# Kernel optimization log

Hardware: AMD Instinct MI355X
Metric: run time of the kernel (lower is better)

The kernel has to match this reference:

```python
import jax, jax.numpy as jnp
import numpy as np

N, E, IN_CH, HID, HEADS, OUT = 50000, 400000, 256, 128, 4, 2
EPS = 1e-5

def _bn(x, g, b):
    # training-mode BatchNorm1d (biased variance), dropout treated as eval (off)
    m = jnp.mean(x, axis=0)
    v = jnp.mean((x - m) ** 2, axis=0)
    return (x - m) * jax.lax.rsqrt(v + EPS) * g + b

def _sage(x, src, dst, Wl, bl, Wr):
    # PyG SAGEConv: lin_l(mean_{j->i} x_j) + lin_r(x_i)
    msg = jax.ops.segment_sum(x[src], dst, num_segments=N)
    deg = jax.ops.segment_sum(jnp.ones((src.shape[0],), x.dtype), dst, num_segments=N)
    agg = msg / jnp.maximum(deg, 1.0)[:, None]
    return agg @ Wl.T + bl + x @ Wr.T

def _gat(x, src, dst, W, a_s, a_d, bias):
    # PyG GATConv with self-loops already appended to (src, dst); concat heads
    d = W.shape[0] // HEADS
    xh = (x @ W.T).reshape(N, HEADS, d)
    asrc = jnp.einsum('nhd,hd->nh', xh, a_s)
    adst = jnp.einsum('nhd,hd->nh', xh, a_d)
    e = jax.nn.leaky_relu(asrc[src] + adst[dst], 0.2)          # [E+N, H]
    m = jax.ops.segment_max(e, dst, num_segments=N)            # segment softmax
    ex = jnp.exp(e - m[dst])
    den = jax.ops.segment_sum(ex, dst, num_segments=N)
    alpha = ex / den[dst]
    out = jax.ops.segment_sum(alpha[:, :, None] * xh[src], dst, num_segments=N)
    return out.reshape(N, HEADS * d) + bias

def setup_inputs():
    key = jax.random.key(0)
    ks = jax.random.split(key, 12)
    rnd = lambda k, s: jax.random.normal(k, s, dtype=jnp.float32) * 0.05
    H4 = HID * HEADS
    return {
        'x': jax.random.normal(ks[0], (N, IN_CH), dtype=jnp.float32),
        'edge_index': jax.random.randint(ks[1], (2, E), 0, N, dtype=jnp.int32),
        'W1l': rnd(ks[2], (HID, IN_CH)), 'b1': jnp.zeros((HID,), jnp.float32),
        'W1r': rnd(ks[3], (HID, IN_CH)),
        'g1': jnp.ones((HID,), jnp.float32), 'be1': jnp.zeros((HID,), jnp.float32),
        'Wg': rnd(ks[4], (H4, HID)),
        'a_src': rnd(ks[5], (HEADS, HID)), 'a_dst': rnd(ks[6], (HEADS, HID)),
        'gbias': jnp.zeros((H4,), jnp.float32),
        'g2': jnp.ones((H4,), jnp.float32), 'be2': jnp.zeros((H4,), jnp.float32),
        'W2l': rnd(ks[7], (HID, H4)), 'b2': jnp.zeros((HID,), jnp.float32),
        'W2r': rnd(ks[8], (HID, H4)),
        'g3': jnp.ones((HID,), jnp.float32), 'be3': jnp.zeros((HID,), jnp.float32),
        'Wf1': rnd(ks[9], (HID // 2, HID)), 'bf1': jnp.zeros((HID // 2,), jnp.float32),
        'g4': jnp.ones((HID // 2,), jnp.float32), 'be4': jnp.zeros((HID // 2,), jnp.float32),
        'Wf2': rnd(ks[10], (OUT, HID // 2)), 'bf2': jnp.zeros((OUT,), jnp.float32),
    }

def reference(x, edge_index, W1l, b1, W1r, g1, be1, Wg, a_src, a_dst, gbias,
              g2, be2, W2l, b2, W2r, g3, be3, Wf1, bf1, g4, be4, Wf2, bf2):
    src, dst = edge_index[0], edge_index[1]
    h = jax.nn.elu(_bn(_sage(x, src, dst, W1l, b1, W1r), g1, be1))
    loop = jnp.arange(N, dtype=src.dtype)                      # GAT adds self-loops
    src_sl = jnp.concatenate([src, loop])
    dst_sl = jnp.concatenate([dst, loop])
    h = jax.nn.elu(_bn(_gat(h, src_sl, dst_sl, Wg, a_src, a_dst, gbias), g2, be2))
    h = jax.nn.elu(_bn(_sage(h, src, dst, W2l, b2, W2r), g3, be3))
    h = jax.nn.elu(_bn(h @ Wf1.T + bf1, g4, be4))
    return h @ Wf2.T + bf2
```

## Files before the change

kernel.cpp:

```cpp
#include <hip/hip_runtime.h>
#include <cstdint>
#include <cstddef>

#define NN 50000
#define EE 400000
#define BN_EPS 1e-5f
#define NB_SCAN 196
#define NWAVE 8192
#define GB 784
#define GAGG 2048
#define G2 64

typedef __attribute__((ext_vector_type(8))) short s16x8;
typedef __attribute__((ext_vector_type(4))) float floatx4;

__device__ __forceinline__ unsigned short f2b(float f) {
    uint32_t u = __float_as_uint(f);
    uint32_t r = (u + 0x7fffu + ((u >> 16) & 1u)) >> 16;
    return (unsigned short)r;
}
__device__ __forceinline__ uint32_t pack2(float a, float b) {
    return (uint32_t)f2b(a) | ((uint32_t)f2b(b) << 16);
}
__device__ __forceinline__ float b2f_lo(uint32_t u) { return __uint_as_float(u << 16); }
__device__ __forceinline__ float b2f_hi(uint32_t u) { return __uint_as_float(u & 0xffff0000u); }

#define GLD16(g, l) __builtin_amdgcn_global_load_lds(                          \
    (const __attribute__((address_space(1))) uint32_t*)(g),                    \
    (__attribute__((address_space(3))) uint32_t*)(l), 16, 0, 0)

__global__ __launch_bounds__(256)
void gemm_w256(const unsigned short* __restrict__ A,
               const unsigned short* __restrict__ W,
               unsigned short* __restrict__ Cb, float* __restrict__ Cf,
               int M, int K)
{
    __shared__ __align__(16) unsigned short As[128 * 32];
    __shared__ __align__(16) unsigned short Bs[256 * 32];
    const int t  = threadIdx.x;
    const int m0 = blockIdx.x * 128;
    const int lane = t & 63;
    const int lr = lane & 15;
    const int lq = lane >> 4;
    const int wid = t >> 6;
    const int wr  = (wid >> 1) * 64;
    const int wc2 = (wid & 1) * 128;

    floatx4 acc[4][8];
    const floatx4 zero = {0.f, 0.f, 0.f, 0.f};
    #pragma unroll
    for (int i = 0; i < 4; ++i)
        #pragma unroll
        for (int j = 0; j < 8; ++j) acc[i][j] = zero;

    for (int k0 = 0; k0 < K; k0 += 32) {
        #pragma unroll
        for (int it = 0; it < 2; ++it) {
            const int seg  = t + it * 256;
            const int row  = seg >> 2;
            const int klog = (seg & 3) ^ ((row >> 1) & 3);
            const unsigned short* ga = A + (size_t)min(m0 + row, M - 1) * K + k0 + klog * 8;
            GLD16(ga, As + seg * 8);
        }
        #pragma unroll
        for (int it = 0; it < 4; ++it) {
            const int seg  = t + it * 256;
            const int row  = seg >> 2;
            const int klog = (seg & 3) ^ ((row >> 1) & 3);
            const unsigned short* gb = W + (size_t)row * K + k0 + klog * 8;
            GLD16(gb, Bs + seg * 8);
        }
        __syncthreads();

        s16x8 af[4], bf[8];
        #pragma unroll
        for (int i = 0; i < 4; ++i) {
            const int ra = wr + i * 16 + lr;
            const int pa = lq ^ ((ra >> 1) & 3);
            af[i] = *(const s16x8*)(As + (ra * 4 + pa) * 8);
        }
        #pragma unroll
        for (int j = 0; j < 8; ++j) {
            const int rb = wc2 + j * 16 + lr;
            const int pb = lq ^ ((rb >> 1) & 3);
            bf[j] = *(const s16x8*)(Bs + (rb * 4 + pb) * 8);
        }
        #pragma unroll
        for (int i = 0; i < 4; ++i)
            #pragma unroll
            for (int j = 0; j < 8; ++j)
                acc[i][j] = __builtin_amdgcn_mfma_f32_16x16x32_bf16(
                    bf[j], af[i], acc[i][j], 0, 0, 0);
        __syncthreads();
    }

    const int orow = lane & 15;
    const int oc4  = (lane >> 4) * 4;
    #pragma unroll
    for (int i = 0; i < 4; ++i) {
        const int r = m0 + wr + i * 16 + orow;
        if (r >= M) continue;
        if (wc2 == 0) {
            #pragma unroll
            for (int j = 0; j < 8; ++j) {
                const int c = j * 16 + oc4;
                const floatx4 a = acc[i][j];
                uint2 ov;
                ov.x = pack2(a[0], a[1]);
                ov.y = pack2(a[2], a[3]);
                *(uint2*)(Cb + (size_t)r * 128 + c) = ov;
            }
        } else {
            #pragma unroll
            for (int j = 0; j < 8; ++j) {
                const int c = j * 16 + oc4;
                const floatx4 a = acc[i][j];
                *(float4*)(Cf + (size_t)r * 128 + c) = make_float4(a[0], a[1], a[2], a[3]);
            }
        }
    }
}

__global__ __launch_bounds__(256)
void gemm_bf16mm(const unsigned short* __restrict__ A,
                 const unsigned short* __restrict__ W,
                 const float* __restrict__ bias,
                 unsigned short* __restrict__ Cb, float* __restrict__ Cf,
                 int split, int M, int K, int Ncol, int ldb, int ldf)
{
    __shared__ __align__(16) unsigned short As[128 * 32];
    __shared__ __align__(16) unsigned short Bs[128 * 32];
    const int t  = threadIdx.x;
    const int m0 = blockIdx.y * 128;
    const int n0 = blockIdx.x * 128;
    const int lane = t & 63;
    const int lr = lane & 15;
    const int lq = lane >> 4;
    const int wr = (t >> 7) * 64;
    const int wc = ((t >> 6) & 1) * 64;

    floatx4 acc[4][4];
    const floatx4 zero = {0.f, 0.f, 0.f, 0.f};
    #pragma unroll
    for (int i = 0; i < 4; ++i)
        #pragma unroll
        for (int j = 0; j < 4; ++j) acc[i][j] = zero;

    for (int k0 = 0; k0 < K; k0 += 32) {
        #pragma unroll
        for (int it = 0; it < 2; ++it) {
            const int seg  = t + it * 256;
            const int row  = seg >> 2;
            const int klog = (seg & 3) ^ ((row >> 1) & 3);
            const unsigned short* ga = A + (size_t)min(m0 + row, M - 1) * K + k0 + klog * 8;
            GLD16(ga, As + seg * 8);
            const unsigned short* gb = W + (size_t)min(n0 + row, Ncol - 1) * K + k0 + klog * 8;
            GLD16(gb, Bs + seg * 8);
        }
        __syncthreads();

        s16x8 af[4], bf[4];
        #pragma unroll
        for (int i = 0; i < 4; ++i) {
            const int ra = wr + i * 16 + lr;
            const int pa = lq ^ ((ra >> 1) & 3);
            af[i] = *(const s16x8*)(As + (ra * 4 + pa) * 8);
            const int rb = wc + i * 16 + lr;
            const int pb = lq ^ ((rb >> 1) & 3);
            bf[i] = *(const s16x8*)(Bs + (rb * 4 + pb) * 8);
        }
        #pragma unroll
        for (int i = 0; i < 4; ++i)
            #pragma unroll
            for (int j = 0; j < 4; ++j)
                acc[i][j] = __builtin_amdgcn_mfma_f32_16x16x32_bf16(
                    bf[j], af[i], acc[i][j], 0, 0, 0);
        __syncthreads();
    }

    const int orow = lane & 15;
    const int oc4  = (lane >> 4) * 4;
    #pragma unroll
    for (int i = 0; i < 4; ++i) {
        const int r = m0 + wr + i * 16 + orow;
        if (r >= M) continue;
        #pragma unroll
        for (int j = 0; j < 4; ++j) {
            const int cb = n0 + wc + j * 16 + oc4;
            if (cb >= Ncol) continue;
            const floatx4 a = acc[i][j];
            if (cb < split) {
                uint2 ov;
                ov.x = pack2(a[0], a[1]);
                ov.y = pack2(a[2], a[3]);
                *(uint2*)(Cb + (size_t)r * ldb + cb) = ov;
            } else {
                const int cc = cb - split;
                float4 o = make_float4(a[0], a[1], a[2], a[3]);
                if (bias) {
                    o.x += bias[cc]; o.y += bias[cc + 1];
                    o.z += bias[cc + 2]; o.w += bias[cc + 3];
                }
                *(float4*)(Cf + (size_t)r * ldf + cc) = o;
            }
        }
    }
}

__global__ __launch_bounds__(256)
void gemm_heads(const unsigned short* __restrict__ agg,
                const unsigned short* __restrict__ Wg,
                const float* __restrict__ gbias,
                unsigned short* __restrict__ out)
{
    __shared__ __align__(16) unsigned short As[128 * 32];
    __shared__ __align__(16) unsigned short Bs[128 * 32];
    const int t  = threadIdx.x;
    const int m0 = blockIdx.x * 128;
    const int h  = blockIdx.y;
    const int lane = t & 63;
    const int lr = lane & 15;
    const int lq = lane >> 4;
    const int wr = (t >> 7) * 64;
    const int wc = ((t >> 6) & 1) * 64;

    floatx4 acc[4][4];
    const floatx4 zero = {0.f, 0.f, 0.f, 0.f};
    #pragma unroll
    for (int i = 0; i < 4; ++i)
        #pragma unroll
        for (int j = 0; j < 4; ++j) acc[i][j] = zero;

    for (int k0 = 0; k0 < 128; k0 += 32) {
        #pragma unroll
        for (int it = 0; it < 2; ++it) {
            const int seg  = t + it * 256;
            const int row  = seg >> 2;
            const int klog = (seg & 3) ^ ((row >> 1) & 3);
            const unsigned short* ga = agg + (size_t)min(m0 + row, NN - 1) * 512 + h * 128 + k0 + klog * 8;
            GLD16(ga, As + seg * 8);
            const unsigned short* gb = Wg + (size_t)(h * 128 + row) * 128 + k0 + klog * 8;
            GLD16(gb, Bs + seg * 8);
        }
        __syncthreads();

        s16x8 af[4], bf[4];
        #pragma unroll
        for (int i = 0; i < 4; ++i) {
            const int ra = wr + i * 16 + lr;
            const int pa = lq ^ ((ra >> 1) & 3);
            af[i] = *(const s16x8*)(As + (ra * 4 + pa) * 8);
            const int rb = wc + i * 16 + lr;
            const int pb = lq ^ ((rb >> 1) & 3);
            bf[i] = *(const s16x8*)(Bs + (rb * 4 + pb) * 8);
        }
        #pragma unroll
        for (int i = 0; i < 4; ++i)
            #pragma unroll
            for (int j = 0; j < 4; ++j)
                acc[i][j] = __builtin_amdgcn_mfma_f32_16x16x32_bf16(
                    bf[j], af[i], acc[i][j], 0, 0, 0);
        __syncthreads();
    }

    const int orow = lane & 15;
    const int oc4  = (lane >> 4) * 4;
    #pragma unroll
    for (int i = 0; i < 4; ++i) {
        const int r = m0 + wr + i * 16 + orow;
        if (r >= NN) continue;
        #pragma unroll
        for (int j = 0; j < 4; ++j) {
            const int c = wc + j * 16 + oc4;
            const floatx4 a = acc[i][j];
            const float* gb = gbias + h * 128 + c;
            uint2 ov;
            ov.x = pack2(a[0] + gb[0], a[1] + gb[1]);
            ov.y = pack2(a[2] + gb[2], a[3] + gb[3]);
            *(uint2*)(out + (size_t)r * 512 + h * 128 + c) = ov;
        }
    }
}

__global__ void k_conv_x(const float* __restrict__ x, unsigned short* __restrict__ xb)
{
    const int i8 = (blockIdx.x * 256 + threadIdx.x) * 8;
    const float4 f0 = *(const float4*)(x + i8);
    const float4 f1 = *(const float4*)(x + i8 + 4);
    uint4 o;
    o.x = pack2(f0.x, f0.y); o.y = pack2(f0.z, f0.w);
    o.z = pack2(f1.x, f1.y); o.w = pack2(f1.z, f1.w);
    *(uint4*)(xb + i8) = o;
}

__global__ void k_conv_w(const float* __restrict__ s0, const float* __restrict__ s1,
                         const float* __restrict__ s2, const float* __restrict__ s3,
                         const float* __restrict__ s4, const float* __restrict__ s5,
                         unsigned short* __restrict__ dst)
{
    const int i = blockIdx.x * 256 + threadIdx.x;
    if (i >= 270336) return;
    float v;
    if      (i < 32768)  v = s0[i];
    else if (i < 65536)  v = s1[i - 32768];
    else if (i < 131072) v = s2[i - 65536];
    else if (i < 196608) v = s3[i - 131072];
    else if (i < 262144) v = s4[i - 196608];
    else                 v = s5[i - 262144];
    dst[i] = f2b(v);
}

__global__ void k_atilde(const float* __restrict__ a_s, const float* __restrict__ a_d,
                         const float* __restrict__ Wg, float* __restrict__ ats,
                         float* __restrict__ atd)
{
    const int k = threadIdx.x;
    const int h = blockIdx.x;
    float s = 0.f, d = 0.f;
    for (int j = 0; j < 128; ++j) {
        const float w = Wg[(size_t)(h * 128 + j) * 128 + k];
        s += a_s[h * 128 + j] * w;
        d += a_d[h * 128 + j] * w;
    }
    ats[h * 128 + k] = s;
    atd[h * 128 + k] = d;
}

__global__ void k_count(const int* __restrict__ dst, int* __restrict__ cnt)
{
    int i = blockIdx.x * blockDim.x + threadIdx.x;
    if (i < EE) atomicAdd(&cnt[dst[i]], 1);
}

__global__ __launch_bounds__(256)
void k_scan_blk(const int* __restrict__ cnt, int* __restrict__ offs,
                int* __restrict__ bsum, int N)
{
    __shared__ int wsum[4];
    const int t = threadIdx.x;
    const int i = blockIdx.x * 256 + t;
    const int v = (i < N) ? cnt[i] : 0;
    int s = v;
    #pragma unroll
    for (int o = 1; o < 64; o <<= 1) {
        const int u = __shfl_up(s, o);
        if ((t & 63) >= o) s += u;
    }
    const int wid = t >> 6;
    if ((t & 63) == 63) wsum[wid] = s;
    __syncthreads();
    int base = 0;
    #pragma unroll
    for (int w = 0; w < 3; ++w) if (w < wid) base += wsum[w];
    if (i < N) offs[i] = base + s - v;
    if (t == 255) bsum[blockIdx.x] = base + s;
}

__global__ __launch_bounds__(256)
void k_scan_top(int* __restrict__ bsum, int* __restrict__ offs, int N)
{
    __shared__ int wsum[4];
    const int t = threadIdx.x;
    const int v = (t < NB_SCAN) ? bsum[t] : 0;
    int s = v;
    #pragma unroll
    for (int o = 1; o < 64; o <<= 1) {
        const int u = __shfl_up(s, o);
        if ((t & 63) >= o) s += u;
    }
    const int wid = t >> 6;
    if ((t & 63) == 63) wsum[wid] = s;
    __syncthreads();
    int base = 0;
    #pragma unroll
    for (int w = 0; w < 3; ++w) if (w < wid) base += wsum[w];
    if (t < NB_SCAN) bsum[t] = base + s - v;
    if (t == 255) offs[N] = base + s;
}

__global__ __launch_bounds__(256)
void k_scan_add(int* __restrict__ offs, const int* __restrict__ bsum, int N)
{
    const int i = blockIdx.x * 256 + threadIdx.x;
    if (i < N) offs[i] += bsum[blockIdx.x];
}

__global__ void k_fill(const int* __restrict__ src, const int* __restrict__ dst,
                       const int* __restrict__ offs, int* __restrict__ fill,
                       int* __restrict__ csr)
{
    int i = blockIdx.x * blockDim.x + threadIdx.x;
    if (i < EE) {
        int d = dst[i];
        int p = offs[d] + atomicAdd(&fill[d], 1);
        csr[p] = src[i];
    }
}

__global__ __launch_bounds__(256)
void k_sage_agg(const unsigned short* __restrict__ tl, float* __restrict__ tr,
                const float* __restrict__ bias, const int* __restrict__ offs,
                const int* __restrict__ csr, float* __restrict__ P)
{
    __shared__ float red[4][256];
    const int l  = threadIdx.x & 63;
    const int g  = l >> 4;
    const int c0 = (l & 15) * 8;
    const int wid = threadIdx.x >> 6;
    const int wv = blockIdx.x * 4 + wid;
    const float4 bv0 = *(const float4*)(bias + c0);
    const float4 bv1 = *(const float4*)(bias + c0 + 4);
    float ps[8] = {0.f,0.f,0.f,0.f,0.f,0.f,0.f,0.f};
    float qs[8] = {0.f,0.f,0.f,0.f,0.f,0.f,0.f,0.f};
    for (int nb = wv * 4; nb < NN; nb += NWAVE * 4) {
        const int n = nb + g;
        if (n < NN) {
            const int o0 = offs[n];
            const int deg = offs[n + 1] - o0;
            float a[8] = {0.f,0.f,0.f,0.f,0.f,0.f,0.f,0.f};
            for (int j = 0; j < deg; ++j) {
                const int sid = csr[o0 + j];
                const uint4 q = *(const uint4*)(tl + (size_t)sid * 128 + c0);
                a[0] += b2f_lo(q.x); a[1] += b2f_hi(q.x);
                a[2] += b2f_lo(q.y); a[3] += b2f_hi(q.y);
                a[4] += b2f_lo(q.z); a[5] += b2f_hi(q.z);
                a[6] += b2f_lo(q.w); a[7] += b2f_hi(q.w);
            }
            const float inv = 1.f / fmaxf((float)deg, 1.f);
            float* tp = tr + (size_t)n * 128 + c0;
            float4 t0 = *(float4*)tp;
            float4 t1 = *(float4*)(tp + 4);
            float v[8];
            v[0] = t0.x + a[0] * inv + bv0.x; v[1] = t0.y + a[1] * inv + bv0.y;
            v[2] = t0.z + a[2] * inv + bv0.z; v[3] = t0.w + a[3] * inv + bv0.w;
            v[4] = t1.x + a[4] * inv + bv1.x; v[5] = t1.y + a[5] * inv + bv1.y;
            v[6] = t1.z + a[6] * inv + bv1.z; v[7] = t1.w + a[7] * inv + bv1.w;
            *(float4*)tp       = make_float4(v[0], v[1], v[2], v[3]);
            *(float4*)(tp + 4) = make_float4(v[4], v[5], v[6], v[7]);
            #pragma unroll
            for (int i = 0; i < 8; ++i) { ps[i] += v[i]; qs[i] += v[i] * v[i]; }
        }
    }
    #pragma unroll
    for (int i = 0; i < 8; ++i) {
        ps[i] += __shfl_xor(ps[i], 16); ps[i] += __shfl_xor(ps[i], 32);
        qs[i] += __shfl_xor(qs[i], 16); qs[i] += __shfl_xor(qs[i], 32);
    }
    if (l < 16) {
        #pragma unroll
        for (int i = 0; i < 8; ++i) {
            red[wid][c0 + i]       = ps[i];
            red[wid][128 + c0 + i] = qs[i];
        }
    }
    __syncthreads();
    const int tc = threadIdx.x;
    const float s = red[0][tc] + red[1][tc] + red[2][tc] + red[3][tc];
    P[(size_t)blockIdx.x * 256 + tc] = s;
}

__global__ __launch_bounds__(256)
void k_attn_agg(const unsigned short* __restrict__ h1, const float* __restrict__ asrc,
                const float* __restrict__ adst, const int* __restrict__ offs,
                const int* __restrict__ csr, unsigned short* __restrict__ agg)
{
    const int l  = threadIdx.x & 63;
    const int g  = l >> 4;
    const int c0 = (l & 15) * 8;
    const int wv = blockIdx.x * 4 + (threadIdx.x >> 6);
    for (int nb = wv * 4; nb < NN; nb += NWAVE * 4) {
        const int n = nb + g;
        if (n >= NN) continue;
        const int o0 = offs[n];
        const int deg = offs[n + 1] - o0;
        const int total = deg + 1;
        const float4 adv = *(const float4*)(adst + n * 4);
        float den0 = 0.f, den1 = 0.f, den2 = 0.f, den3 = 0.f;
        float acc[4][8];
        #pragma unroll
        for (int h = 0; h < 4; ++h)
            #pragma unroll
            for (int i = 0; i < 8; ++i) acc[h][i] = 0.f;
        for (int j = 0; j < total; ++j) {
            const int sid = (j < deg) ? csr[o0 + j] : n;
            const float4 av = *(const float4*)(asrc + sid * 4);
            float e0 = av.x + adv.x, e1 = av.y + adv.y;
            float e2 = av.z + adv.z, e3 = av.w + adv.w;
            e0 = fmaxf(e0, 0.2f * e0); e1 = fmaxf(e1, 0.2f * e1);
            e2 = fmaxf(e2, 0.2f * e2); e3 = fmaxf(e3, 0.2f * e3);
            const float w0 = __expf(e0), w1 = __expf(e1);
            const float w2 = __expf(e2), w3 = __expf(e3);
            den0 += w0; den1 += w1; den2 += w2; den3 += w3;
            const uint4 q = *(const uint4*)(h1 + (size_t)sid * 128 + c0);
            float v[8];
            v[0] = b2f_lo(q.x); v[1] = b2f_hi(q.x);
            v[2] = b2f_lo(q.y); v[3] = b2f_hi(q.y);
            v[4] = b2f_lo(q.z); v[5] = b2f_hi(q.z);
            v[6] = b2f_lo(q.w); v[7] = b2f_hi(q.w);
            #pragma unroll
            for (int i = 0; i < 8; ++i) {
                acc[0][i] += w0 * v[i];
                acc[1][i] += w1 * v[i];
                acc[2][i] += w2 * v[i];
                acc[3][i] += w3 * v[i];
            }
        }
        const float r[4] = {1.f / den0, 1.f / den1, 1.f / den2, 1.f / den3};
        #pragma unroll
        for (int h = 0; h < 4; ++h) {
            uint4 ov;
            ov.x = pack2(acc[h][0] * r[h], acc[h][1] * r[h]);
            ov.y = pack2(acc[h][2] * r[h], acc[h][3] * r[h]);
            ov.z = pack2(acc[h][4] * r[h], acc[h][5] * r[h]);
            ov.w = pack2(acc[h][6] * r[h], acc[h][7] * r[h]);
            *(uint4*)(agg + (size_t)n * 512 + h * 128 + c0) = ov;
        }
    }
}

__global__ __launch_bounds__(256)
void k_statsA_b2(const unsigned short* __restrict__ X, float* __restrict__ P)
{
    const int c = threadIdx.x * 2;
    const int b = blockIdx.x;
    const int r0 = b * 64;
    const int r1 = min(r0 + 64, NN);
    float s0 = 0.f, s1 = 0.f, q0 = 0.f, q1 = 0.f;
    for (int r = r0; r < r1; ++r) {
        const uint32_t u = *(const uint32_t*)(X + (size_t)r * 512 + c);
        const float v0 = b2f_lo(u), v1 = b2f_hi(u);
        s0 += v0; q0 += v0 * v0;
        s1 += v1; q1 += v1 * v1;
    }
    *(float2*)(P + (size_t)b * 1024 + c) = make_float2(s0, s1);
    *(float2*)(P + (size_t)b * 1024 + 512 + c) = make_float2(q0, q1);
}

__global__ __launch_bounds__(64)
void k_statsA_f(const float* __restrict__ X, float* __restrict__ P)
{
    const int c = threadIdx.x;
    const int b = blockIdx.x;
    const int r0 = b * 64;
    const int r1 = min(r0 + 64, NN);
    float s = 0.f, q = 0.f;
    for (int r = r0; r < r1; ++r) {
        const float v = X[(size_t)r * 64 + c];
        s += v; q += v * v;
    }
    P[(size_t)b * 128 + c] = s;
    P[(size_t)b * 128 + 64 + c] = q;
}

__global__ __launch_bounds__(256)
void k_red1(const float* __restrict__ P, float* __restrict__ P2, int C2, int nb)
{
    const int g = blockIdx.x;
    for (int c = threadIdx.x; c < C2; c += 256) {
        float s = 0.f;
        for (int b = g; b < nb; b += G2) s += P[(size_t)b * C2 + c];
        P2[(size_t)g * C2 + c] = s;
    }
}

template<int CHUNK>
__global__ void k_bn_reduce(const float* __restrict__ P, int C, int nb,
                            const float* __restrict__ g, const float* __restrict__ be,
                            float* __restrict__ scale, float* __restrict__ shift)
{
    __shared__ float sb[8 * CHUNK];
    __shared__ float qb[8 * CHUNK];
    const int t = threadIdx.x;
    const int cl = t & (CHUNK - 1);
    const int grp = t / CHUNK;
    const int c = blockIdx.x * CHUNK + cl;
    float s = 0.f, q = 0.f;
    for (int b = grp; b < nb; b += 8) {
        s += P[(size_t)b * 2 * C + c];
        q += P[(size_t)b * 2 * C + C + c];
    }
    sb[grp * CHUNK + cl] = s;
    qb[grp * CHUNK + cl] = q;
    __syncthreads();
    if (t < CHUNK) {
        float S = 0.f, Q = 0.f;
        #pragma unroll
        for (int g2 = 0; g2 < 8; ++g2) { S += sb[g2 * CHUNK + t]; Q += qb[g2 * CHUNK + t]; }
        const int cc = blockIdx.x * CHUNK + t;
        const float mean = S / (float)NN;
        float var = Q / (float)NN - mean * mean;
        var = fmaxf(var, 0.f);
        const float sc = g[cc] * rsqrtf(var + BN_EPS);
        scale[cc] = sc;
        shift[cc] = be[cc] - mean * sc;
    }
}

__global__ void k_bn_elu_f2b(const float* __restrict__ X, unsigned short* __restrict__ D,
                             const float* __restrict__ scale, const float* __restrict__ shift,
                             int Cm1, int total)
{
    const int i = (blockIdx.x * 256 + threadIdx.x) * 4;
    if (i >= total) return;
    const int c = i & Cm1;
    const float4 x = *(const float4*)(X + i);
    float o[4] = {x.x, x.y, x.z, x.w};
    #pragma unroll
    for (int k = 0; k < 4; ++k) {
        const float v = o[k] * scale[c + k] + shift[c + k];
        o[k] = (v > 0.f) ? v : (__expf(v) - 1.f);
    }
    uint2 ov;
    ov.x = pack2(o[0], o[1]); ov.y = pack2(o[2], o[3]);
    *(uint2*)(D + i) = ov;
}

__global__ void k_bn_elu_b2b(unsigned short* __restrict__ X,
                             const float* __restrict__ scale, const float* __restrict__ shift,
                             int Cm1, int total)
{
    const int i = (blockIdx.x * 256 + threadIdx.x) * 4;
    if (i >= total) return;
    const int c = i & Cm1;
    const uint2 u = *(const uint2*)(X + i);
    float o[4] = {b2f_lo(u.x), b2f_hi(u.x), b2f_lo(u.y), b2f_hi(u.y)};
    #pragma unroll
    for (int k = 0; k < 4; ++k) {
        const float v = o[k] * scale[c + k] + shift[c + k];
        o[k] = (v > 0.f) ? v : (__expf(v) - 1.f);
    }
    uint2 ov;
    ov.x = pack2(o[0], o[1]); ov.y = pack2(o[2], o[3]);
    *(uint2*)(X + i) = ov;
}

__global__ __launch_bounds__(256)
void k_bn_elu_coef(const float* __restrict__ X, unsigned short* __restrict__ D,
                   const float* __restrict__ scale, const float* __restrict__ shift,
                   const float* __restrict__ ats, const float* __restrict__ atd,
                   float* __restrict__ asrc, float* __restrict__ adst)
{
    const int l = threadIdx.x & 63;
    const int wv = blockIdx.x * 4 + (threadIdx.x >> 6);
    const int c = l * 2;
    const float2 sc = *(const float2*)(scale + c);
    const float2 sh = *(const float2*)(shift + c);
    float2 sa[4], da[4];
    #pragma unroll
    for (int h = 0; h < 4; ++h) {
        sa[h] = *(const float2*)(ats + h * 128 + c);
        da[h] = *(const float2*)(atd + h * 128 + c);
    }
    for (int n = wv; n < NN; n += NWAVE) {
        const float2 xv = *(const float2*)(X + (size_t)n * 128 + c);
        float v0 = xv.x * sc.x + sh.x;
        float v1 = xv.y * sc.y + sh.y;
        v0 = (v0 > 0.f) ? v0 : (__expf(v0) - 1.f);
        v1 = (v1 > 0.f) ? v1 : (__expf(v1) - 1.f);
        const uint32_t p = pack2(v0, v1);
        *(uint32_t*)(D + (size_t)n * 128 + c) = p;
        const float r0 = b2f_lo(p), r1 = b2f_hi(p);
        float ps[4], pd[4];
        #pragma unroll
        for (int h = 0; h < 4; ++h) {
            ps[h] = r0 * sa[h].x + r1 * sa[h].y;
            pd[h] = r0 * da[h].x + r1 * da[h].y;
        }
        #pragma unroll
        for (int o = 1; o < 64; o <<= 1) {
            #pragma unroll
            for (int h = 0; h < 4; ++h) {
                ps[h] += __shfl_xor(ps[h], o);
                pd[h] += __shfl_xor(pd[h], o);
            }
        }
        if (l == 0) {
            *(float4*)(asrc + n * 4) = make_float4(ps[0], ps[1], ps[2], ps[3]);
            *(float4*)(adst + n * 4) = make_float4(pd[0], pd[1], pd[2], pd[3]);
        }
    }
}

__global__ __launch_bounds__(256)
void k_bn_elu_fc2(const float* __restrict__ X, const float* __restrict__ scale,
                  const float* __restrict__ shift, const float* __restrict__ W,
                  const float* __restrict__ bias, float* __restrict__ out)
{
    const int c = threadIdx.x & 63;
    const int gw = blockIdx.x * 4 + (threadIdx.x >> 6);
    const float sc = scale[c], sh = shift[c];
    const float w0 = W[c], w1 = W[64 + c];
    const float b0 = bias[0], b1 = bias[1];
    for (int n = gw; n < NN; n += NWAVE) {
        float v = X[(size_t)n * 64 + c] * sc + sh;
        v = (v > 0.f) ? v : (__expf(v) - 1.f);
        float p0 = v * w0;
        float p1 = v * w1;
        #pragma unroll
        for (int o = 1; o < 64; o <<= 1) {
            p0 += __shfl_xor(p0, o);
            p1 += __shfl_xor(p1, o);
        }
        if (c == 0) {
            out[n * 2 + 0] = p0 + b0;
            out[n * 2 + 1] = p1 + b1;
        }
    }
}

extern "C" void kernel_launch(void* const* d_in, const int* in_sizes, int n_in,
                              void* d_out, int out_size, void* d_ws, size_t ws_size,
                              hipStream_t stream)
{
    const float* x     = (const float*)d_in[0];
    const int*   ei    = (const int*)d_in[1];
    const float* W1l   = (const float*)d_in[2];
    const float* b1    = (const float*)d_in[3];
    const float* W1r   = (const float*)d_in[4];
    const float* g1    = (const float*)d_in[5];
    const float* be1   = (const float*)d_in[6];
    const float* Wg    = (const float*)d_in[7];
    const float* a_s   = (const float*)d_in[8];
    const float* a_d   = (const float*)d_in[9];
    const float* gbias = (const float*)d_in[10];
    const float* g2    = (const float*)d_in[11];
    const float* be2   = (const float*)d_in[12];
    const float* W2l   = (const float*)d_in[13];
    const float* b2    = (const float*)d_in[14];
    const float* W2r   = (const float*)d_in[15];
    const float* g3    = (const float*)d_in[16];
    const float* be3   = (const float*)d_in[17];
    const float* Wf1   = (const float*)d_in[18];
    const float* bf1   = (const float*)d_in[19];
    const float* g4    = (const float*)d_in[20];
    const float* be4   = (const float*)d_in[21];
    const float* Wf2   = (const float*)d_in[22];
    const float* bf2   = (const float*)d_in[23];
    const int* src = ei;
    const int* dst = ei + EE;

    char* ws = (char*)d_ws;
    size_t off = 0;
    auto alloc = [&](size_t bytes) -> char* {
        char* p = ws + off;
        off += (bytes + 255) & ~(size_t)255;
        return p;
    };
    unsigned short* xb   = (unsigned short*)alloc((size_t)NN * 256 * 2);
    unsigned short* waren= (unsigned short*)alloc(270336 * 2);
    unsigned short* tlb  = (unsigned short*)alloc((size_t)NN * 128 * 2);
    float*          trF  = (float*)alloc((size_t)NN * 128 * 4);
    unsigned short* h1b  = (unsigned short*)alloc((size_t)NN * 128 * 2);
    unsigned short* aggb = (unsigned short*)alloc((size_t)NN * 512 * 2);
    unsigned short* gatb = (unsigned short*)alloc((size_t)NN * 512 * 2);
    float* asrc  = (float*)alloc((size_t)NN * 4 * 4);
    float* adst  = (float*)alloc((size_t)NN * 4 * 4);
    float* ats   = (float*)alloc(512 * 4);
    float* atd   = (float*)alloc(512 * 4);
    float* pstat = (float*)alloc((size_t)GAGG * 256 * 4 > (size_t)GB * 1024 * 4
                                 ? (size_t)GAGG * 256 * 4 : (size_t)GB * 1024 * 4);
    float* pstat2= (float*)alloc((size_t)G2 * 1024 * 4);
    float* scsh  = (float*)alloc(1024 * 4);
    int*   cntfill = (int*)alloc((size_t)NN * 2 * 4);
    int*   offs  = (int*)alloc((size_t)(NN + 1) * 4);
    int*   csr   = (int*)alloc((size_t)EE * 4);
    int*   bsum  = (int*)alloc((size_t)NB_SCAN * 4);
    if (off > ws_size) return;
    (void)in_sizes; (void)n_in; (void)out_size;

    unsigned short* W1cat = waren;
    unsigned short* Wg_b  = waren + 65536;
    unsigned short* W2cat = waren + 131072;
    unsigned short* Wf1_b = waren + 262144;

    int* cnt  = cntfill;
    int* fill = cntfill + NN;
    float* scale = scsh;
    float* shift = scsh + 512;

    k_conv_x<<<6250, 256, 0, stream>>>(x, xb);
    k_conv_w<<<1056, 256, 0, stream>>>(W1l, W1r, Wg, W2l, W2r, Wf1, waren);
    k_atilde<<<4, 128, 0, stream>>>(a_s, a_d, Wg, ats, atd);
    hipMemsetAsync(cntfill, 0, (size_t)NN * 2 * 4, stream);
    k_count<<<(EE + 255) / 256, 256, 0, stream>>>(dst, cnt);
    k_scan_blk<<<NB_SCAN, 256, 0, stream>>>(cnt, offs, bsum, NN);
    k_scan_top<<<1, 256, 0, stream>>>(bsum, offs, NN);
    k_scan_add<<<NB_SCAN, 256, 0, stream>>>(offs, bsum, NN);
    k_fill<<<(EE + 255) / 256, 256, 0, stream>>>(src, dst, offs, fill, csr);

    const int gy = (NN + 127) / 128;

    gemm_w256<<<gy, 256, 0, stream>>>(xb, W1cat, tlb, trF, NN, 256);
    k_sage_agg<<<GAGG, 256, 0, stream>>>(tlb, trF, b1, offs, csr, pstat);
    k_red1<<<G2, 256, 0, stream>>>(pstat, pstat2, 256, GAGG);
    k_bn_reduce<128><<<1, 1024, 0, stream>>>(pstat2, 128, G2, g1, be1, scale, shift);
    k_bn_elu_coef<<<2048, 256, 0, stream>>>(trF, h1b, scale, shift, ats, atd, asrc, adst);

    k_attn_agg<<<2048, 256, 0, stream>>>(h1b, asrc, adst, offs, csr, aggb);
    gemm_heads<<<dim3(gy, 4), 256, 0, stream>>>(aggb, Wg_b, gbias, gatb);
    k_statsA_b2<<<GB, 256, 0, stream>>>(gatb, pstat);
    k_red1<<<G2, 256, 0, stream>>>(pstat, pstat2, 1024, GB);
    k_bn_reduce<128><<<4, 1024, 0, stream>>>(pstat2, 512, G2, g2, be2, scale, shift);
    k_bn_elu_b2b<<<(NN * 512 / 4 + 255) / 256, 256, 0, stream>>>(gatb, scale, shift, 511, NN * 512);

    gemm_w256<<<gy, 256, 0, stream>>>(gatb, W2cat, tlb, trF, NN, 512);
    k_sage_agg<<<GAGG, 256, 0, stream>>>(tlb, trF, b2, offs, csr, pstat);
    k_red1<<<G2, 256, 0, stream>>>(pstat, pstat2, 256, GAGG);
    k_bn_reduce<128><<<1, 1024, 0, stream>>>(pstat2, 128, G2, g3, be3, scale, shift);
    k_bn_elu_f2b<<<(NN * 128 / 4 + 255) / 256, 256, 0, stream>>>(trF, h1b, scale, shift, 127, NN * 128);

    gemm_bf16mm<<<dim3(1, gy), 256, 0, stream>>>(h1b, Wf1_b, bf1, nullptr, trF,
                                                 0, NN, 128, 64, 0, 64);
    k_statsA_f<<<GB, 64, 0, stream>>>(trF, pstat);
    k_red1<<<G2, 256, 0, stream>>>(pstat, pstat2, 128, GB);
    k_bn_reduce<64><<<1, 512, 0, stream>>>(pstat2, 64, G2, g4, be4, scale, shift);

    k_bn_elu_fc2<<<2048, 256, 0, stream>>>(trF, scale, shift, Wf2, bf2, (float*)d_out);
}
```

Baseline: 540.5 us.

## Fuse GAT BN statistics into gemm_heads epilogue and unroll gather loops by two

The GAT output GEMM now computes per-column sum and sum-of-squares in its epilogue, using wave shuffles and shared memory, and writes per-block partials. This removes the separate k_statsA_b2 pass that re-read the 50000x512 bf16 output. The statistics come from fp32 values before bf16 rounding, which differs slightly from the old path. Separately, the SAGE and attention gather loops are unrolled by two so two neighbour-row loads are in flight at once, raising memory-level parallelism at some register cost. The pstat buffer is shrunk because only the GAGG-sized partials are needed now.

```diff
diff --git a/kernel.cpp b/kernel.cpp
--- a/kernel.cpp
+++ b/kernel.cpp
@@ -211,16 +211,19 @@
 void gemm_heads(const unsigned short* __restrict__ agg,
                 const unsigned short* __restrict__ Wg,
                 const float* __restrict__ gbias,
-                unsigned short* __restrict__ out)
+                unsigned short* __restrict__ out, float* __restrict__ P)
 {
     __shared__ __align__(16) unsigned short As[128 * 32];
     __shared__ __align__(16) unsigned short Bs[128 * 32];
+    __shared__ float sred[4][64];
+    __shared__ float qred[4][64];
     const int t  = threadIdx.x;
     const int m0 = blockIdx.x * 128;
     const int h  = blockIdx.y;
     const int lane = t & 63;
     const int lr = lane & 15;
     const int lq = lane >> 4;
+    const int wid = t >> 6;
     const int wr = (t >> 7) * 64;
     const int wc = ((t >> 6) & 1) * 64;
 
@@ -265,20 +268,58 @@
 
     const int orow = lane & 15;
     const int oc4  = (lane >> 4) * 4;
+    float cs[16], cq[16];
+    #pragma unroll
+    for (int z = 0; z < 16; ++z) { cs[z] = 0.f; cq[z] = 0.f; }
     #pragma unroll
     for (int i = 0; i < 4; ++i) {
         const int r = m0 + wr + i * 16 + orow;
-        if (r >= NN) continue;
+        const bool ok = (r < NN);
         #pragma unroll
         for (int j = 0; j < 4; ++j) {
             const int c = wc + j * 16 + oc4;
             const floatx4 a = acc[i][j];
             const float* gb = gbias + h * 128 + c;
-            uint2 ov;
-            ov.x = pack2(a[0] + gb[0], a[1] + gb[1]);
-            ov.y = pack2(a[2] + gb[2], a[3] + gb[3]);
-            *(uint2*)(out + (size_t)r * 512 + h * 128 + c) = ov;
-        }
+            float v0 = a[0] + gb[0], v1 = a[1] + gb[1];
+            float v2 = a[2] + gb[2], v3 = a[3] + gb[3];
+            if (ok) {
+                uint2 ov;
+                ov.x = pack2(v0, v1);
+                ov.y = pack2(v2, v3);
+                *(uint2*)(out + (size_t)r * 512 + h * 128 + c) = ov;
+                cs[j*4+0] += v0; cq[j*4+0] += v0 * v0;
+                cs[j*4+1] += v1; cq[j*4+1] += v1 * v1;
+                cs[j*4+2] += v2; cq[j*4+2] += v2 * v2;
+                cs[j*4+3] += v3; cq[j*4+3] += v3 * v3;
+            }
+        }
+    }
+    #pragma unroll
+    for (int z = 0; z < 16; ++z) {
+        #pragma unroll
+        for (int o = 1; o < 16; o <<= 1) {
+            cs[z] += __shfl_xor(cs[z], o);
+            cq[z] += __shfl_xor(cq[z], o);
+        }
+    }
+    if ((lane & 15) == 0) {
+        #pragma unroll
+        for (int j = 0; j < 4; ++j)
+            #pragma unroll
+            for (int k = 0; k < 4; ++k) {
+                sred[wid][j * 16 + oc4 + k] = cs[j*4+k];
+                qred[wid][j * 16 + oc4 + k] = cq[j*4+k];
+            }
+    }
+    __syncthreads();
+    {
+        const int cc  = t & 127;
+        const int isq = t >> 7;
+        const int wA  = (cc < 64) ? 0 : 1;
+        const int ci  = cc & 63;
+        const float val = isq ? (qred[wA][ci] + qred[wA + 2][ci])
+                              : (sred[wA][ci] + sred[wA + 2][ci]);
+        P[(size_t)blockIdx.x * 1024 + isq * 512 + h * 128 + cc] = val;
     }
 }
 
@@ -416,15 +457,31 @@
         const int n = nb + g;
         if (n < NN) {
             const int o0 = offs[n];
-            const int deg = offs[n + 1] - o0;
+            const int o1 = offs[n + 1];
+            const int deg = o1 - o0;
             float a[8] = {0.f,0.f,0.f,0.f,0.f,0.f,0.f,0.f};
-            for (int j = 0; j < deg; ++j) {
-                const int sid = csr[o0 + j];
-                const uint4 q = *(const uint4*)(tl + (size_t)sid * 128 + c0);
-                a[0] += b2f_lo(q.x); a[1] += b2f_hi(q.x);
-                a[2] += b2f_lo(q.y); a[3] += b2f_hi(q.y);
-                a[4] += b2f_lo(q.z); a[5] += b2f_hi(q.z);
-                a[6] += b2f_lo(q.w); a[7] += b2f_hi(q.w);
+            int j = o0;
+            for (; j + 1 < o1; j += 2) {
+                const int s0 = csr[j];
+                const int s1 = csr[j + 1];
+                const uint4 q0 = *(const uint4*)(tl + (size_t)s0 * 128 + c0);
+                const uint4 q1 = *(const uint4*)(tl + (size_t)s1 * 128 + c0);
+                a[0] += b2f_lo(q0.x); a[1] += b2f_hi(q0.x);
+                a[2] += b2f_lo(q0.y); a[3] += b2f_hi(q0.y);
+                a[4] += b2f_lo(q0.z); a[5] += b2f_hi(q0.z);
+                a[6] += b2f_lo(q0.w); a[7] += b2f_hi(q0.w);
+                a[0] += b2f_lo(q1.x); a[1] += b2f_hi(q1.x);
+                a[2] += b2f_lo(q1.y); a[3] += b2f_hi(q1.y);
+                a[4] += b2f_lo(q1.z); a[5] += b2f_hi(q1.z);
+                a[6] += b2f_lo(q1.w); a[7] += b2f_hi(q1.w);
+            }
+            if (j < o1) {
+                const int s0 = csr[j];
+                const uint4 q0 = *(const uint4*)(tl + (size_t)s0 * 128 + c0);
+                a[0] += b2f_lo(q0.x); a[1] += b2f_hi(q0.x);
+                a[2] += b2f_lo(q0.y); a[3] += b2f_hi(q0.y);
+                a[4] += b2f_lo(q0.z); a[5] += b2f_hi(q0.z);
+                a[6] += b2f_lo(q0.w); a[7] += b2f_hi(q0.w);
             }
             const float inv = 1.f / fmaxf((float)deg, 1.f);
             float* tp = tr + (size_t)n * 128 + c0;
@@ -481,9 +538,49 @@
         for (int h = 0; h < 4; ++h)
             #pragma unroll
             for (int i = 0; i < 8; ++i) acc[h][i] = 0.f;
-        for (int j = 0; j < total; ++j) {
+        int j = 0;
+        for (; j + 1 < total; j += 2) {
+            const int sidA = (j < deg) ? csr[o0 + j] : n;
+            const int sidB = (j + 1 < deg) ? csr[o0 + j + 1] : n;
+            const float4 avA = *(const float4*)(asrc + sidA * 4);
+            const float4 avB = *(const float4*)(asrc + sidB * 4);
+            const uint4 qA = *(const uint4*)(h1 + (size_t)sidA * 128 + c0);
+            const uint4 qB = *(const uint4*)(h1 + (size_t)sidB * 128 + c0);
+            float eA0 = avA.x + adv.x, eA1 = avA.y + adv.y;
+            float eA2 = avA.z + adv.z, eA3 = avA.w + adv.w;
+            eA0 = fmaxf(eA0, 0.2f * eA0); eA1 = fmaxf(eA1, 0.2f * eA1);
+            eA2 = fmaxf(eA2, 0.2f * eA2); eA3 = fmaxf(eA3, 0.2f * eA3);
+            const float wA0 = __expf(eA0), wA1 = __expf(eA1);
+            const float wA2 = __expf(eA2), wA3 = __expf(eA3);
+            float eB0 = avB.x + adv.x, eB1 = avB.y + adv.y;
+            float eB2 = avB.z + adv.z, eB3 = avB.w + adv.w;
+            eB0 = fmaxf(eB0, 0.2f * eB0); eB1 = fmaxf(eB1, 0.2f * eB1);
+            eB2 = fmaxf(eB2, 0.2f * eB2); eB3 = fmaxf(eB3, 0.2f * eB3);
+            const float wB0 = __expf(eB0), wB1 = __expf(eB1);
+            const float wB2 = __expf(eB2), wB3 = __expf(eB3);
+            den0 += wA0 + wB0; den1 += wA1 + wB1;
+            den2 += wA2 + wB2; den3 += wA3 + wB3;
+            float vA[8], vB[8];
+            vA[0] = b2f_lo(qA.x); vA[1] = b2f_hi(qA.x);
+            vA[2] = b2f_lo(qA.y); vA[3] = b2f_hi(qA.y);
+            vA[4] = b2f_lo(qA.z); vA[5] = b2f_hi(qA.z);
+            vA[6] = b2f_lo(qA.w); vA[7] = b2f_hi(qA.w);
+            vB[0] = b2f_lo(qB.x); vB[1] = b2f_hi(qB.x);
+            vB[2] = b2f_lo(qB.y); vB[3] = b2f_hi(qB.y);
+            vB[4] = b2f_lo(qB.z); vB[5] = b2f_hi(qB.z);
+            vB[6] = b2f_lo(qB.w); vB[7] = b2f_hi(qB.w);
+            #pragma unroll
+            for (int i = 0; i < 8; ++i) {
+                acc[0][i] += wA0 * vA[i] + wB0 * vB[i];
+                acc[1][i] += wA1 * vA[i] + wB1 * vB[i];
+                acc[2][i] += wA2 * vA[i] + wB2 * vB[i];
+                acc[3][i] += wA3 * vA[i] + wB3 * vB[i];
+            }
+        }
+        if (j < total) {
             const int sid = (j < deg) ? csr[o0 + j] : n;
             const float4 av = *(const float4*)(asrc + sid * 4);
+            const uint4 q = *(const uint4*)(h1 + (size_t)sid * 128 + c0);
             float e0 = av.x + adv.x, e1 = av.y + adv.y;
             float e2 = av.z + adv.z, e3 = av.w + adv.w;
             e0 = fmaxf(e0, 0.2f * e0); e1 = fmaxf(e1, 0.2f * e1);
@@ -491,7 +588,6 @@
             const float w0 = __expf(e0), w1 = __expf(e1);
             const float w2 = __expf(e2), w3 = __expf(e3);
             den0 += w0; den1 += w1; den2 += w2; den3 += w3;
-            const uint4 q = *(const uint4*)(h1 + (size_t)sid * 128 + c0);
             float v[8];
             v[0] = b2f_lo(q.x); v[1] = b2f_hi(q.x);
             v[2] = b2f_lo(q.y); v[3] = b2f_hi(q.y);
@@ -516,24 +612,6 @@
             *(uint4*)(agg + (size_t)n * 512 + h * 128 + c0) = ov;
         }
     }
-}
-
-__global__ __launch_bounds__(256)
-void k_statsA_b2(const unsigned short* __restrict__ X, float* __restrict__ P)
-{
-    const int c = threadIdx.x * 2;
-    const int b = blockIdx.x;
-    const int r0 = b * 64;
-    const int r1 = min(r0 + 64, NN);
-    float s0 = 0.f, s1 = 0.f, q0 = 0.f, q1 = 0.f;
-    for (int r = r0; r < r1; ++r) {
-        const uint32_t u = *(const uint32_t*)(X + (size_t)r * 512 + c);
-        const float v0 = b2f_lo(u), v1 = b2f_hi(u);
-        s0 += v0; q0 += v0 * v0;
-        s1 += v1; q1 += v1 * v1;
-    }
-    *(float2*)(P + (size_t)b * 1024 + c) = make_float2(s0, s1);
-    *(float2*)(P + (size_t)b * 1024 + 512 + c) = make_float2(q0, q1);
 }
 
 __global__ __launch_bounds__(64)
@@ -757,8 +835,7 @@
     float* adst  = (float*)alloc((size_t)NN * 4 * 4);
     float* ats   = (float*)alloc(512 * 4);
     float* atd   = (float*)alloc(512 * 4);
-    float* pstat = (float*)alloc((size_t)GAGG * 256 * 4 > (size_t)GB * 1024 * 4
-                                 ? (size_t)GAGG * 256 * 4 : (size_t)GB * 1024 * 4);
+    float* pstat = (float*)alloc((size_t)GAGG * 256 * 4);
     float* pstat2= (float*)alloc((size_t)G2 * 1024 * 4);
     float* scsh  = (float*)alloc(1024 * 4);
     int*   cntfill = (int*)alloc((size_t)NN * 2 * 4);
@@ -797,9 +874,8 @@
     k_bn_elu_coef<<<2048, 256, 0, stream>>>(trF, h1b, scale, shift, ats, atd, asrc, adst);
 
     k_attn_agg<<<2048, 256, 0, stream>>>(h1b, asrc, adst, offs, csr, aggb);
-    gemm_heads<<<dim3(gy, 4), 256, 0, stream>>>(aggb, Wg_b, gbias, gatb);
-    k_statsA_b2<<<GB, 256, 0, stream>>>(gatb, pstat);
-    k_red1<<<G2, 256, 0, stream>>>(pstat, pstat2, 1024, GB);
+    gemm_heads<<<dim3(gy, 4), 256, 0, stream>>>(aggb, Wg_b, gbias, gatb, pstat);
+    k_red1<<<G2, 256, 0, stream>>>(pstat, pstat2, 1024, gy);
     k_bn_reduce<128><<<4, 1024, 0, stream>>>(pstat2, 512, G2, g2, be2, scale, shift);
     k_bn_elu_b2b<<<(NN * 512 / 4 + 255) / 256, 256, 0, stream>>>(gatb, scale, shift, 511, NN * 512);
 
```

Result: no change. 548.4 us (+1.5%).
